# Performance work log

Hardware: AMD Instinct MI355X
Metric: run time of the kernel (lower is better)

The kernel has to match this reference:

```python
import jax, jax.numpy as jnp
import numpy as np

NUM_HEADS = 16

def _rope_tables(seq_len, head_dim, dtype):
    inv_freq = 1.0 / (10000.0 ** (jnp.arange(0, head_dim, 2, dtype=jnp.float32) / head_dim))
    t = jnp.arange(seq_len, dtype=jnp.float32)
    freqs = jnp.einsum('i,j->ij', t, inv_freq)          # [S, hd/2]
    emb = jnp.concatenate([freqs, freqs], axis=-1)      # [S, hd]
    return jnp.cos(emb).astype(dtype), jnp.sin(emb).astype(dtype)

def _rotate_half(x):
    x1, x2 = jnp.split(x, 2, axis=-1)
    return jnp.concatenate([-x2, x1], axis=-1)

def _apply_rope(x, cos, sin):
    # x: [B, H, S, hd]; cos/sin: [S, hd]
    return x * cos + _rotate_half(x) * sin

def setup_inputs() -> dict:
    key = jax.random.key(0)
    ks = jax.random.split(key, 9)
    S, B, E = 2048, 2, 1024
    sc_w = 1.0 / np.sqrt(E)
    inp = {
        'query': jax.random.normal(ks[0], (S, B, E), jnp.float32),
        'wq': jax.random.normal(ks[1], (E, E), jnp.float32) * sc_w,
        'bq': jax.random.normal(ks[2], (E,), jnp.float32) * 0.02,
        'wk': jax.random.normal(ks[3], (E, E), jnp.float32) * sc_w,
        'bk': jax.random.normal(ks[4], (E,), jnp.float32) * 0.02,
        'wv': jax.random.normal(ks[5], (E, E), jnp.float32) * sc_w,
        'bv': jax.random.normal(ks[6], (E,), jnp.float32) * 0.02,
        'wo': jax.random.normal(ks[7], (E, E), jnp.float32) * sc_w,
        'bo': jax.random.normal(ks[8], (E,), jnp.float32) * 0.02,
    }
    return inp

def reference(query, wq, bq, wk, bk, wv, bv, wo, bo):
    S, B, E = query.shape
    H = NUM_HEADS
    hd = E // H
    # QKV projections (torch Linear: x @ W^T + b). self_attention => k,v from query.
    q = jnp.einsum('sbe,fe->sbf', query, wq) + bq
    k = jnp.einsum('sbe,fe->sbf', query, wk) + bk
    v = jnp.einsum('sbe,fe->sbf', query, wv) + bv
    # [S, B, E] -> [B, H, S, hd]
    def to_bhsd(x):
        return x.reshape(S, B, H, hd).transpose(1, 2, 0, 3)
    q, k, v = to_bhsd(q), to_bhsd(k), to_bhsd(v)
    cos, sin = _rope_tables(S, hd, query.dtype)
    q = _apply_rope(q, cos, sin)
    k = _apply_rope(k, cos, sin)
    # scaled dot-product attention (no mask, no dropout)
    scale = 1.0 / jnp.sqrt(jnp.asarray(hd, query.dtype))
    scores = jnp.einsum('bhqd,bhkd->bhqk', q, k) * scale
    probs = jax.nn.softmax(scores, axis=-1)
    attn = jnp.einsum('bhqk,bhkd->bhqd', probs, v)
    # [B, H, S, hd] -> [S, B, E]
    attn = attn.transpose(2, 0, 1, 3).reshape(S, B, E)
    out = jnp.einsum('sbe,fe->sbf', attn, wo) + bo
    return out
```

## Files before the change

### kernel.cpp

```cpp
#include <hip/hip_runtime.h>
#include <stdint.h>

#define S_LEN 2048
#define BATCH 2
#define EMB   1024
#define NHEAD 16
#define HDIM  64

typedef __bf16 bf8   __attribute__((ext_vector_type(8)));
typedef float  f32x4 __attribute__((ext_vector_type(4)));
typedef float  f32x16 __attribute__((ext_vector_type(16)));

__device__ __forceinline__ unsigned short f2bf(float f) {
    unsigned u = __builtin_bit_cast(unsigned, f);
    u += 0x7fffu + ((u >> 16) & 1u);
    return (unsigned short)(u >> 16);
}
__device__ __forceinline__ float bf2f(unsigned short h) {
    unsigned u = ((unsigned)h) << 16;
    return __builtin_bit_cast(float, u);
}

__device__ __forceinline__ void gl_lds16(const unsigned short* g, unsigned short* l) {
    __builtin_amdgcn_global_load_lds(
        (__attribute__((address_space(1))) void*)(void*)g,
        (__attribute__((address_space(3))) void*)(void*)l, 16, 0, 0);
}

__global__ void k_tables(float* __restrict__ cosT, float* __restrict__ sinT) {
    int idx = blockIdx.x * 256 + threadIdx.x;
    int s = idx >> 6, d = idx & 63, j = d & 31;
    float inv = exp2f(-13.28771237954945f * ((float)j * (1.0f / 32.0f)));
    float ang = (float)s * inv;
    cosT[idx] = cosf(ang);
    sinT[idx] = sinf(ang);
}

__global__ void k_cast_x(const float* __restrict__ x, unsigned short* __restrict__ xb) {
    int id = blockIdx.x * 256 + threadIdx.x;
    int b = id >> 19, rem = id & 524287;
    int s = rem >> 8, e4 = (rem & 255) << 2;
    float4 v = *(const float4*)&x[((size_t)(s * BATCH + b)) * EMB + e4];
    ushort4 o;
    o.x = f2bf(v.x); o.y = f2bf(v.y); o.z = f2bf(v.z); o.w = f2bf(v.w);
    *(ushort4*)&xb[((size_t)(b * S_LEN + s)) * EMB + e4] = o;
}

__global__ void k_castW(const float* __restrict__ w0, const float* __restrict__ w1,
                        const float* __restrict__ w2, const float* __restrict__ w3,
                        unsigned short* __restrict__ o0, unsigned short* __restrict__ o1,
                        unsigned short* __restrict__ o2, unsigned short* __restrict__ o3) {
    int id = blockIdx.x * 256 + threadIdx.x;
    int seg = id >> 18, r = id & 262143;
    const float* s = seg == 0 ? w0 : seg == 1 ? w1 : seg == 2 ? w2 : w3;
    unsigned short* o = seg == 0 ? o0 : seg == 1 ? o1 : seg == 2 ? o2 : o3;
    float4 v = *(const float4*)&s[(size_t)r * 4];
    ushort4 u;
    u.x = f2bf(v.x); u.y = f2bf(v.y); u.z = f2bf(v.z); u.w = f2bf(v.w);
    *(ushort4*)&o[(size_t)r * 4] = u;
}

__global__ void __launch_bounds__(256) k_gemmQKV(
    const unsigned short* __restrict__ A,
    const unsigned short* __restrict__ Wq, const unsigned short* __restrict__ Wk,
    const unsigned short* __restrict__ Wv,
    const float* __restrict__ bqp, const float* __restrict__ bkp, const float* __restrict__ bvp,
    unsigned short* __restrict__ qout, unsigned short* __restrict__ kout,
    unsigned short* __restrict__ vout,
    const float* __restrict__ cosT, const float* __restrict__ sinT)
{
    __shared__ __align__(16) unsigned short As[128 * 32];
    __shared__ __align__(16) unsigned short Bs[128 * 32];
    const int z = blockIdx.z;
    const unsigned short* B = z == 0 ? Wq : z == 1 ? Wk : Wv;
    const float* bias = z == 0 ? bqp : z == 1 ? bkp : bvp;
    const int tid  = threadIdx.x;
    const int lane = tid & 63;
    const int wid  = tid >> 6;
    const int wm = wid >> 1, wn = wid & 1;
    const int l15 = lane & 15, lh = lane >> 4;
    const int tm0 = blockIdx.y * 128, tn0 = blockIdx.x * 128;
    const int K = 1024;

    f32x4 acc[4][4] = {};

    for (int k0 = 0; k0 < K; k0 += 32) {
        __syncthreads();
#pragma unroll
        for (int rnd = 0; rnd < 2; ++rnd) {
            int cbase = wid * 64 + rnd * 256;
            int c = cbase + lane;
            int row = c >> 2, co = (c & 3) * 8;
            gl_lds16(A + (size_t)(tm0 + row) * K + k0 + co, &As[cbase * 8]);
            gl_lds16(B + (size_t)(tn0 + row) * K + k0 + co, &Bs[cbase * 8]);
        }
        __syncthreads();
        bf8 a[4], b[4];
#pragma unroll
        for (int i = 0; i < 4; ++i) {
            a[i] = *(const bf8*)&As[(wm * 64 + i * 16 + l15) * 32 + lh * 8];
            b[i] = *(const bf8*)&Bs[(wn * 64 + i * 16 + l15) * 32 + lh * 8];
        }
#pragma unroll
        for (int i = 0; i < 4; ++i)
#pragma unroll
            for (int j = 0; j < 4; ++j)
                acc[i][j] = __builtin_amdgcn_mfma_f32_16x16x32_bf16(a[i], b[j], acc[i][j], 0, 0, 0);
    }

    if (z < 2) {
        unsigned short* C = z ? kout : qout;
        const float f = z ? 1.0f : 0.125f * 1.44269504089f;
#pragma unroll
        for (int i = 0; i < 4; ++i) {
            const int rowb = tm0 + wm * 64 + i * 16 + lh * 4;
#pragma unroll
            for (int j = 0; j < 2; ++j) {
                const int col = tn0 + wn * 64 + j * 16 + l15;
                const int d = j * 16 + l15;
#pragma unroll
                for (int r = 0; r < 4; ++r) {
                    int m = rowb + r;
                    int sq = m & (S_LEN - 1);
                    float x1 = acc[i][j][r]     + bias[col];
                    float x2 = acc[i][j + 2][r] + bias[col + 32];
                    float c  = cosT[sq * 64 + d] * f;
                    float sn = sinT[sq * 64 + d] * f;
                    C[(size_t)m * EMB + col]      = f2bf(x1 * c - x2 * sn);
                    C[(size_t)m * EMB + col + 32] = f2bf(x2 * c + x1 * sn);
                }
            }
        }
    } else {
#pragma unroll
        for (int i = 0; i < 4; ++i) {
            const int rowb = tm0 + wm * 64 + i * 16 + lh * 4;
#pragma unroll
            for (int j = 0; j < 4; ++j) {
                const int col = tn0 + wn * 64 + j * 16 + l15;
                float bv = bias[col];
#pragma unroll
                for (int r = 0; r < 4; ++r)
                    vout[(size_t)col * 4096 + rowb + r] = f2bf(acc[i][j][r] + bv);
            }
        }
    }
}

__global__ void __launch_bounds__(256) k_attn6(
    const unsigned short* __restrict__ qb,
    const unsigned short* __restrict__ kb,
    const unsigned short* __restrict__ vT,
    float* __restrict__ po0, float* __restrict__ po1,
    float* __restrict__ ml)
{
    __shared__ __align__(16) unsigned short Kl[2][4096];
    __shared__ __align__(16) unsigned short Vl[2][4096];
    __shared__ float bl[4][32];
    const int tid = threadIdx.x, lane = tid & 63, wid = tid >> 6;
    const int l31 = lane & 31, hi = lane >> 5;
    const int bh = blockIdx.y;
    const int b = bh >> 4, h = bh & 15;
    const int z = blockIdx.z;
    const int kv0 = z << 10;
    const int q0 = blockIdx.x * 128 + wid * 32;
    float* __restrict__ po = z ? po1 : po0;
    float* __restrict__ mlz = ml + (size_t)z * (32 * 2048 * 2);

    const unsigned short* qrow = qb + ((size_t)(b * S_LEN + q0 + l31)) * EMB + h * HDIM + hi * 8;
    bf8 qf[4];
#pragma unroll
    for (int c = 0; c < 4; ++c) qf[c] = *(const bf8*)(qrow + c * 16);

    const unsigned short* kb_g = kb + (size_t)b * S_LEN * EMB + h * HDIM;
    const unsigned short* vT_g = vT + (size_t)h * HDIM * (S_LEN * BATCH) + b * S_LEN;

    const int srow = lane >> 3;
    const int sp   = lane & 7;
    auto stage = [&](int buf, int j0) {
#pragma unroll
        for (int i = 0; i < 2; ++i) {
            int blk = wid * 2 + i;
            int r = blk * 8 + srow;
            int ps = sp ^ (r & 7);
            gl_lds16(kb_g + (size_t)(j0 + r) * EMB + ps * 8, &Kl[buf][blk * 512]);
            gl_lds16(vT_g + (size_t)r * (S_LEN * BATCH) + j0 + ps * 8, &Vl[buf][blk * 512]);
        }
    };

    auto pack2 = [](float lo, float hh) -> unsigned {
        unsigned short a  = __builtin_bit_cast(unsigned short, (__bf16)lo);
        unsigned short bb = __builtin_bit_cast(unsigned short, (__bf16)hh);
        return ((unsigned)bb << 16) | a;
    };

    float m_run = 0.f, l_run = 0.f;
    f32x16 oacc0 = {}, oacc1 = {};

    const int rA = l31, rB = 32 + l31;

    stage(0, kv0);
    __syncthreads();

    const int NT = 1024 / 64;
    for (int t = 0; t < NT; ++t) {
        const int cur = t & 1;
        if (t < NT - 1) stage(cur ^ 1, kv0 + (t + 1) * 64);

        f32x16 stA = {}, stB = {};
#pragma unroll
        for (int c = 0; c < 4; ++c) {
            int s = c * 2 + hi;
            bf8 kfa = *(const bf8*)&Kl[cur][rA * 64 + (s ^ (rA & 7)) * 8];
            bf8 kfb = *(const bf8*)&Kl[cur][rB * 64 + (s ^ (rB & 7)) * 8];
            stA = __builtin_amdgcn_mfma_f32_32x32x16_bf16(kfa, qf[c], stA, 0, 0, 0);
            stB = __builtin_amdgcn_mfma_f32_32x32x16_bf16(kfb, qf[c], stB, 0, 0, 0);
        }
        float mx[8];
#pragma unroll
        for (int i = 0; i < 8; ++i)
            mx[i] = fmaxf(fmaxf(stA[i], stA[i + 8]), fmaxf(stB[i], stB[i + 8]));
        float t0 = fmaxf(mx[0], mx[4]), t1 = fmaxf(mx[1], mx[5]);
        float t2 = fmaxf(mx[2], mx[6]), t3 = fmaxf(mx[3], mx[7]);
        float pmax = fmaxf(fmaxf(t0, t1), fmaxf(t2, t3));
        pmax = fmaxf(pmax, __shfl_xor(pmax, 32));
        if (!__all(pmax - m_run <= 11.54f)) {
            float mnew = fmaxf(m_run, pmax);
            float corr = exp2f(m_run - mnew);
            l_run *= corr;
            m_run = mnew;
            if (hi == 0) bl[wid][l31] = corr;
            asm volatile("s_waitcnt lgkmcnt(0)" ::: "memory");
#pragma unroll
            for (int r = 0; r < 16; ++r) {
                float c2 = bl[wid][(r & 3) + 8 * (r >> 2) + 4 * hi];
                oacc0[r] *= c2;
                oacc1[r] *= c2;
            }
        }
        float pA[16];
#pragma unroll
        for (int r = 0; r < 16; ++r) pA[r] = exp2f(stA[r] - m_run);
        float sA = ((pA[0] + pA[1]) + (pA[2] + pA[3])) + ((pA[4] + pA[5]) + (pA[6] + pA[7]));
        float sA2 = ((pA[8] + pA[9]) + (pA[10] + pA[11])) + ((pA[12] + pA[13]) + (pA[14] + pA[15]));
        unsigned a01 = pack2(pA[0], pA[1]),   a23 = pack2(pA[2], pA[3]);
        unsigned a45 = pack2(pA[4], pA[5]),   a67 = pack2(pA[6], pA[7]);
        unsigned a89 = pack2(pA[8], pA[9]),   aab = pack2(pA[10], pA[11]);
        unsigned acd = pack2(pA[12], pA[13]), aef = pack2(pA[14], pA[15]);
        unsigned rA_ = (unsigned)__shfl_xor((int)(hi ? a01 : a45), 32);
        unsigned rB_ = (unsigned)__shfl_xor((int)(hi ? a23 : a67), 32);
        unsigned rC_ = (unsigned)__shfl_xor((int)(hi ? a89 : acd), 32);
        unsigned rD_ = (unsigned)__shfl_xor((int)(hi ? aab : aef), 32);
        uint4 u0 = hi ? uint4{rA_, rB_, a45, a67} : uint4{a01, a23, rA_, rB_};
        uint4 u1 = hi ? uint4{rC_, rD_, acd, aef} : uint4{a89, aab, rC_, rD_};
        bf8 pf0A = __builtin_bit_cast(bf8, u0);
        bf8 pf1A = __builtin_bit_cast(bf8, u1);
        float pB[16];
#pragma unroll
        for (int r = 0; r < 16; ++r) pB[r] = exp2f(stB[r] - m_run);
        float sB = ((pB[0] + pB[1]) + (pB[2] + pB[3])) + ((pB[4] + pB[5]) + (pB[6] + pB[7]));
        float sB2 = ((pB[8] + pB[9]) + (pB[10] + pB[11])) + ((pB[12] + pB[13]) + (pB[14] + pB[15]));
        unsigned b01 = pack2(pB[0], pB[1]),   b23 = pack2(pB[2], pB[3]);
        unsigned b45 = pack2(pB[4], pB[5]),   b67 = pack2(pB[6], pB[7]);
        unsigned b89 = pack2(pB[8], pB[9]),   bab = pack2(pB[10], pB[11]);
        unsigned bcd = pack2(pB[12], pB[13]), bef = pack2(pB[14], pB[15]);
        unsigned sA_ = (unsigned)__shfl_xor((int)(hi ? b01 : b45), 32);
        unsigned sB_ = (unsigned)__shfl_xor((int)(hi ? b23 : b67), 32);
        unsigned sC_ = (unsigned)__shfl_xor((int)(hi ? b89 : bcd), 32);
        unsigned sD_ = (unsigned)__shfl_xor((int)(hi ? bab : bef), 32);
        uint4 w0 = hi ? uint4{sA_, sB_, b45, b67} : uint4{b01, b23, sA_, sB_};
        uint4 w1 = hi ? uint4{sC_, sD_, bcd, bef} : uint4{b89, bab, sC_, sD_};
        bf8 pf0B = __builtin_bit_cast(bf8, w0);
        bf8 pf1B = __builtin_bit_cast(bf8, w1);

        float psum = (sA + sA2) + (sB + sB2);
        psum += __shfl_xor(psum, 32);
        l_run += psum;

#pragma unroll
        for (int c = 0; c < 4; ++c) {
            int s = c * 2 + hi;
            bf8 v0 = *(const bf8*)&Vl[cur][rA * 64 + (s ^ (rA & 7)) * 8];
            bf8 v1 = *(const bf8*)&Vl[cur][rB * 64 + (s ^ (rB & 7)) * 8];
            bf8 pf = (c == 0) ? pf0A : (c == 1) ? pf1A : (c == 2) ? pf0B : pf1B;
            oacc0 = __builtin_amdgcn_mfma_f32_32x32x16_bf16(pf, v0, oacc0, 0, 0, 0);
            oacc1 = __builtin_amdgcn_mfma_f32_32x32x16_bf16(pf, v1, oacc1, 0, 0, 0);
        }
        __syncthreads();
    }

#pragma unroll
    for (int r = 0; r < 16; ++r) {
        int q = (r & 3) + 8 * (r >> 2) + 4 * hi;
        size_t base = ((size_t)bh * 2048 + q0 + q) * 64 + l31;
        po[base]      = oacc0[r];
        po[base + 32] = oacc1[r];
    }
    if (hi == 0) {
        size_t mi = ((size_t)bh * 2048 + q0 + l31) * 2;
        mlz[mi]     = m_run;
        mlz[mi + 1] = l_run;
    }
}

__global__ void k_comb(const float* __restrict__ po0, const float* __restrict__ po1,
                       const float* __restrict__ ml, unsigned short* __restrict__ ob)
{
    int id = blockIdx.x * 256 + threadIdx.x;
    int d4 = (id & 15) * 4;
    int q  = (id >> 4) & 2047;
    int bh = id >> 15;
    int b = bh >> 4, h = bh & 15;
    size_t mi = ((size_t)bh * 2048 + q) * 2;
    float m0 = ml[mi], l0 = ml[mi + 1];
    float m1 = ml[mi + (size_t)32 * 2048 * 2], l1 = ml[mi + (size_t)32 * 2048 * 2 + 1];
    float m = fmaxf(m0, m1);
    float w0 = exp2f(m0 - m), w1 = exp2f(m1 - m);
    float inv = 1.0f / (l0 * w0 + l1 * w1);
    size_t pi = ((size_t)bh * 2048 + q) * 64 + d4;
    float4 a = *(const float4*)&po0[pi];
    float4 c = *(const float4*)&po1[pi];
    ushort4 o;
    o.x = f2bf((a.x * w0 + c.x * w1) * inv);
    o.y = f2bf((a.y * w0 + c.y * w1) * inv);
    o.z = f2bf((a.z * w0 + c.z * w1) * inv);
    o.w = f2bf((a.w * w0 + c.w * w1) * inv);
    *(ushort4*)&ob[((size_t)(b * S_LEN + q)) * EMB + h * HDIM + d4] = o;
}

template<int EPI, typename OutT>
__global__ void __launch_bounds__(256) k_gemm(
    const unsigned short* __restrict__ A,
    const unsigned short* __restrict__ B,
    const float* __restrict__ bias,
    OutT* __restrict__ C,
    int M, int N, int K)
{
    __shared__ __align__(16) unsigned short As[128 * 32];
    __shared__ __align__(16) unsigned short Bs[128 * 32];
    const int tid  = threadIdx.x;
    const int lane = tid & 63;
    const int wid  = tid >> 6;
    const int wm = wid >> 1, wn = wid & 1;
    const int l15 = lane & 15, lh = lane >> 4;
    const int tm0 = blockIdx.y * 128, tn0 = blockIdx.x * 128;

    f32x4 acc[4][4] = {};

    for (int k0 = 0; k0 < K; k0 += 32) {
        __syncthreads();
#pragma unroll
        for (int rnd = 0; rnd < 2; ++rnd) {
            int cbase = wid * 64 + rnd * 256;
            int c = cbase + lane;
            int row = c >> 2, co = (c & 3) * 8;
            gl_lds16(A + (size_t)(tm0 + row) * K + k0 + co, &As[cbase * 8]);
            gl_lds16(B + (size_t)(tn0 + row) * K + k0 + co, &Bs[cbase * 8]);
        }
        __syncthreads();
        bf8 a[4], b[4];
#pragma unroll
        for (int i = 0; i < 4; ++i) {
            a[i] = *(const bf8*)&As[(wm * 64 + i * 16 + l15) * 32 + lh * 8];
            b[i] = *(const bf8*)&Bs[(wn * 64 + i * 16 + l15) * 32 + lh * 8];
        }
#pragma unroll
        for (int i = 0; i < 4; ++i)
#pragma unroll
            for (int j = 0; j < 4; ++j)
                acc[i][j] = __builtin_amdgcn_mfma_f32_16x16x32_bf16(a[i], b[j], acc[i][j], 0, 0, 0);
    }

#pragma unroll
    for (int i = 0; i < 4; ++i) {
        const int rowb = tm0 + wm * 64 + i * 16 + lh * 4;
#pragma unroll
        for (int j = 0; j < 4; ++j) {
            const int col = tn0 + wn * 64 + j * 16 + l15;
#pragma unroll
            for (int r = 0; r < 4; ++r) {
                float v = acc[i][j][r];
                int row = rowb + r;
                if (EPI == 0) {
                    v += bias[col];
                    C[(size_t)row * N + col] = (OutT)f2bf(v);
                } else {
                    v += bias[col];
                    int bb = row >> 11, ss = row & 2047;
                    ((float*)C)[(size_t)(ss * BATCH + bb) * N + col] = v;
                }
            }
        }
    }
}

extern "C" void kernel_launch(void* const* d_in, const int* in_sizes, int n_in,
                              void* d_out, int out_size, void* d_ws, size_t ws_size,
                              hipStream_t stream)
{
    (void)in_sizes; (void)n_in; (void)out_size; (void)ws_size;
    const float* query = (const float*)d_in[0];
    const float* wq = (const float*)d_in[1];
    const float* bq = (const float*)d_in[2];
    const float* wk = (const float*)d_in[3];
    const float* bk = (const float*)d_in[4];
    const float* wv = (const float*)d_in[5];
    const float* bv = (const float*)d_in[6];
    const float* wo = (const float*)d_in[7];
    const float* bo = (const float*)d_in[8];

    char* ws = (char*)d_ws;
    float*          cosT = (float*)(ws + 0);
    float*          sinT = (float*)(ws + (512 << 10));
    float*          ml   = (float*)(ws + 0);
    unsigned short* xb   = (unsigned short*)(ws + (1  << 20));
    float*          po0  = (float*)(ws + (1  << 20));
    unsigned short* wqb  = (unsigned short*)(ws + (9  << 20));
    unsigned short* wkb  = (unsigned short*)(ws + (11 << 20));
    unsigned short* wvb  = (unsigned short*)(ws + (13 << 20));
    unsigned short* qb   = (unsigned short*)(ws + (17 << 20));
    unsigned short* ob   = qb;
    unsigned short* kb   = (unsigned short*)(ws + (25 << 20));
    unsigned short* vT   = (unsigned short*)(ws + (33 << 20));
    float*          po1  = (float*)(ws + (41 << 20));
    unsigned short* wob  = (unsigned short*)(ws + (57 << 20));

    k_tables<<<512, 256, 0, stream>>>(cosT, sinT);
    k_cast_x<<<4096, 256, 0, stream>>>(query, xb);
    k_castW<<<4096, 256, 0, stream>>>(wq, wk, wv, wo, wqb, wkb, wvb, wob);

    dim3 gq(EMB / 128, (S_LEN * BATCH) / 128, 3);
    k_gemmQKV<<<gq, 256, 0, stream>>>(xb, wqb, wkb, wvb, bq, bk, bv,
                                      qb, kb, vT, cosT, sinT);

    dim3 g3(S_LEN / 128, BATCH * NHEAD, 2);
    k_attn6<<<g3, 256, 0, stream>>>(qb, kb, vT, po0, po1, ml);
    k_comb<<<4096, 256, 0, stream>>>(po0, po1, ml, ob);

    dim3 g1(EMB / 128, (S_LEN * BATCH) / 128);
    k_gemm<1, float><<<g1, 256, 0, stream>>>(ob, wob, bo, (float*)d_out, 4096, 1024, 1024);
}
```

Measured before the change: 184.1 us.

## Triple-buffer K/V staging in attention with vmcnt waits and MFMA priority

Replaces the double-buffered K/V LDS staging with a three-buffer ring. Each iteration waits with a partial vmcnt and one barrier, so two tiles stay in flight and the trailing per-iteration __syncthreads is gone. It also precomputes the swizzled LDS and global offsets, wraps the MFMA groups in s_setprio, and uses the raw hardware exp2 intrinsic in place of exp2f. The cost is more LDS per block (48KB), which may lower occupancy, plus hand-counted wait counts that must match the issued loads.

```diff
diff --git a/kernel.cpp b/kernel.cpp
--- a/kernel.cpp
+++ b/kernel.cpp
@@ -20,6 +20,8 @@
     unsigned u = ((unsigned)h) << 16;
     return __builtin_bit_cast(float, u);
 }
+__device__ __forceinline__ float fexp2(float x) { return __builtin_amdgcn_exp2f(x); }
+__device__ __forceinline__ float f3max(float a, float b, float c) { return fmaxf(fmaxf(a, b), c); }
 
 __device__ __forceinline__ void gl_lds16(const unsigned short* g, unsigned short* l) {
     __builtin_amdgcn_global_load_lds(
@@ -147,15 +149,14 @@
     }
 }
 
-__global__ void __launch_bounds__(256) k_attn6(
+__global__ void __launch_bounds__(256) k_attn8(
     const unsigned short* __restrict__ qb,
     const unsigned short* __restrict__ kb,
     const unsigned short* __restrict__ vT,
     float* __restrict__ po0, float* __restrict__ po1,
     float* __restrict__ ml)
 {
-    __shared__ __align__(16) unsigned short Kl[2][4096];
-    __shared__ __align__(16) unsigned short Vl[2][4096];
+    __shared__ __align__(16) unsigned short Sm[24576];
     __shared__ float bl[4][32];
     const int tid = threadIdx.x, lane = tid & 63, wid = tid >> 6;
     const int l31 = lane & 31, hi = lane >> 5;
@@ -172,21 +173,28 @@
 #pragma unroll
     for (int c = 0; c < 4; ++c) qf[c] = *(const bf8*)(qrow + c * 16);
 
-    const unsigned short* kb_g = kb + (size_t)b * S_LEN * EMB + h * HDIM;
-    const unsigned short* vT_g = vT + (size_t)h * HDIM * (S_LEN * BATCH) + b * S_LEN;
-
-    const int srow = lane >> 3;
-    const int sp   = lane & 7;
-    auto stage = [&](int buf, int j0) {
-#pragma unroll
-        for (int i = 0; i < 2; ++i) {
-            int blk = wid * 2 + i;
-            int r = blk * 8 + srow;
-            int ps = sp ^ (r & 7);
-            gl_lds16(kb_g + (size_t)(j0 + r) * EMB + ps * 8, &Kl[buf][blk * 512]);
-            gl_lds16(vT_g + (size_t)r * (S_LEN * BATCH) + j0 + ps * 8, &Vl[buf][blk * 512]);
-        }
-    };
+    const int mz = l31 & 7;
+    const int koA0 = l31 * 128 + (((0 * 2 + hi) ^ mz) << 4);
+    const int koA1 = l31 * 128 + (((1 * 2 + hi) ^ mz) << 4);
+    const int koA2 = l31 * 128 + (((2 * 2 + hi) ^ mz) << 4);
+    const int koA3 = l31 * 128 + (((3 * 2 + hi) ^ mz) << 4);
+    const char* ldsc = (const char*)Sm;
+
+    const int srow = lane >> 3, sp = lane & 7;
+    const int r0 = wid * 16 + srow,     p0s = sp ^ (r0 & 7);
+    const int r1 = wid * 16 + 8 + srow, p1s = sp ^ (r1 & 7);
+    const int kgo0 = (r0 * EMB + p0s * 8) * 2, kgo1 = (r1 * EMB + p1s * 8) * 2;
+    const int vgo0 = (r0 * (S_LEN * BATCH) + p0s * 8) * 2, vgo1 = (r1 * (S_LEN * BATCH) + p1s * 8) * 2;
+
+    const unsigned short* kS = kb + ((size_t)(b * S_LEN + kv0)) * EMB + h * HDIM;
+    const unsigned short* vS = vT + ((size_t)h * HDIM) * (S_LEN * BATCH) + b * S_LEN + kv0;
+
+#define STAGE8(DBUF) do { \
+    gl_lds16((const unsigned short*)((const char*)kS + kgo0), Sm + (DBUF) * 4096 + wid * 1024); \
+    gl_lds16((const unsigned short*)((const char*)vS + vgo0), Sm + 12288 + (DBUF) * 4096 + wid * 1024); \
+    gl_lds16((const unsigned short*)((const char*)kS + kgo1), Sm + (DBUF) * 4096 + wid * 1024 + 512); \
+    gl_lds16((const unsigned short*)((const char*)vS + vgo1), Sm + 12288 + (DBUF) * 4096 + wid * 1024 + 512); \
+    kS += 64 * EMB; vS += 64; } while (0)
 
     auto pack2 = [](float lo, float hh) -> unsigned {
         unsigned short a  = __builtin_bit_cast(unsigned short, (__bf16)lo);
@@ -196,98 +204,113 @@
 
     float m_run = 0.f, l_run = 0.f;
     f32x16 oacc0 = {}, oacc1 = {};
-
-    const int rA = l31, rB = 32 + l31;
-
-    stage(0, kv0);
-    __syncthreads();
-
-    const int NT = 1024 / 64;
-    for (int t = 0; t < NT; ++t) {
-        const int cur = t & 1;
-        if (t < NT - 1) stage(cur ^ 1, kv0 + (t + 1) * 64);
-
-        f32x16 stA = {}, stB = {};
-#pragma unroll
-        for (int c = 0; c < 4; ++c) {
-            int s = c * 2 + hi;
-            bf8 kfa = *(const bf8*)&Kl[cur][rA * 64 + (s ^ (rA & 7)) * 8];
-            bf8 kfb = *(const bf8*)&Kl[cur][rB * 64 + (s ^ (rB & 7)) * 8];
-            stA = __builtin_amdgcn_mfma_f32_32x32x16_bf16(kfa, qf[c], stA, 0, 0, 0);
-            stB = __builtin_amdgcn_mfma_f32_32x32x16_bf16(kfb, qf[c], stB, 0, 0, 0);
-        }
-        float mx[8];
-#pragma unroll
-        for (int i = 0; i < 8; ++i)
-            mx[i] = fmaxf(fmaxf(stA[i], stA[i + 8]), fmaxf(stB[i], stB[i + 8]));
-        float t0 = fmaxf(mx[0], mx[4]), t1 = fmaxf(mx[1], mx[5]);
-        float t2 = fmaxf(mx[2], mx[6]), t3 = fmaxf(mx[3], mx[7]);
-        float pmax = fmaxf(fmaxf(t0, t1), fmaxf(t2, t3));
-        pmax = fmaxf(pmax, __shfl_xor(pmax, 32));
-        if (!__all(pmax - m_run <= 11.54f)) {
-            float mnew = fmaxf(m_run, pmax);
-            float corr = exp2f(m_run - mnew);
-            l_run *= corr;
-            m_run = mnew;
-            if (hi == 0) bl[wid][l31] = corr;
-            asm volatile("s_waitcnt lgkmcnt(0)" ::: "memory");
-#pragma unroll
-            for (int r = 0; r < 16; ++r) {
-                float c2 = bl[wid][(r & 3) + 8 * (r >> 2) + 4 * hi];
-                oacc0[r] *= c2;
-                oacc1[r] *= c2;
-            }
-        }
-        float pA[16];
-#pragma unroll
-        for (int r = 0; r < 16; ++r) pA[r] = exp2f(stA[r] - m_run);
-        float sA = ((pA[0] + pA[1]) + (pA[2] + pA[3])) + ((pA[4] + pA[5]) + (pA[6] + pA[7]));
-        float sA2 = ((pA[8] + pA[9]) + (pA[10] + pA[11])) + ((pA[12] + pA[13]) + (pA[14] + pA[15]));
-        unsigned a01 = pack2(pA[0], pA[1]),   a23 = pack2(pA[2], pA[3]);
-        unsigned a45 = pack2(pA[4], pA[5]),   a67 = pack2(pA[6], pA[7]);
-        unsigned a89 = pack2(pA[8], pA[9]),   aab = pack2(pA[10], pA[11]);
-        unsigned acd = pack2(pA[12], pA[13]), aef = pack2(pA[14], pA[15]);
-        unsigned rA_ = (unsigned)__shfl_xor((int)(hi ? a01 : a45), 32);
-        unsigned rB_ = (unsigned)__shfl_xor((int)(hi ? a23 : a67), 32);
-        unsigned rC_ = (unsigned)__shfl_xor((int)(hi ? a89 : acd), 32);
-        unsigned rD_ = (unsigned)__shfl_xor((int)(hi ? aab : aef), 32);
-        uint4 u0 = hi ? uint4{rA_, rB_, a45, a67} : uint4{a01, a23, rA_, rB_};
-        uint4 u1 = hi ? uint4{rC_, rD_, acd, aef} : uint4{a89, aab, rC_, rD_};
-        bf8 pf0A = __builtin_bit_cast(bf8, u0);
-        bf8 pf1A = __builtin_bit_cast(bf8, u1);
-        float pB[16];
-#pragma unroll
-        for (int r = 0; r < 16; ++r) pB[r] = exp2f(stB[r] - m_run);
-        float sB = ((pB[0] + pB[1]) + (pB[2] + pB[3])) + ((pB[4] + pB[5]) + (pB[6] + pB[7]));
-        float sB2 = ((pB[8] + pB[9]) + (pB[10] + pB[11])) + ((pB[12] + pB[13]) + (pB[14] + pB[15]));
-        unsigned b01 = pack2(pB[0], pB[1]),   b23 = pack2(pB[2], pB[3]);
-        unsigned b45 = pack2(pB[4], pB[5]),   b67 = pack2(pB[6], pB[7]);
-        unsigned b89 = pack2(pB[8], pB[9]),   bab = pack2(pB[10], pB[11]);
-        unsigned bcd = pack2(pB[12], pB[13]), bef = pack2(pB[14], pB[15]);
-        unsigned sA_ = (unsigned)__shfl_xor((int)(hi ? b01 : b45), 32);
-        unsigned sB_ = (unsigned)__shfl_xor((int)(hi ? b23 : b67), 32);
-        unsigned sC_ = (unsigned)__shfl_xor((int)(hi ? b89 : bcd), 32);
-        unsigned sD_ = (unsigned)__shfl_xor((int)(hi ? bab : bef), 32);
-        uint4 w0 = hi ? uint4{sA_, sB_, b45, b67} : uint4{b01, b23, sA_, sB_};
-        uint4 w1 = hi ? uint4{sC_, sD_, bcd, bef} : uint4{b89, bab, sC_, sD_};
-        bf8 pf0B = __builtin_bit_cast(bf8, w0);
-        bf8 pf1B = __builtin_bit_cast(bf8, w1);
-
-        float psum = (sA + sA2) + (sB + sB2);
-        psum += __shfl_xor(psum, 32);
-        l_run += psum;
-
-#pragma unroll
-        for (int c = 0; c < 4; ++c) {
-            int s = c * 2 + hi;
-            bf8 v0 = *(const bf8*)&Vl[cur][rA * 64 + (s ^ (rA & 7)) * 8];
-            bf8 v1 = *(const bf8*)&Vl[cur][rB * 64 + (s ^ (rB & 7)) * 8];
-            bf8 pf = (c == 0) ? pf0A : (c == 1) ? pf1A : (c == 2) ? pf0B : pf1B;
-            oacc0 = __builtin_amdgcn_mfma_f32_32x32x16_bf16(pf, v0, oacc0, 0, 0, 0);
-            oacc1 = __builtin_amdgcn_mfma_f32_32x32x16_bf16(pf, v1, oacc1, 0, 0, 0);
-        }
-        __syncthreads();
-    }
+    const f32x16 Z16 = {};
+
+    STAGE8(0);
+    STAGE8(1);
+
+#define ABODY(BUF, DOSTG, LASTW) do { \
+    if (LASTW) asm volatile("s_waitcnt vmcnt(0)" ::: "memory"); \
+    else       asm volatile("s_waitcnt vmcnt(4)" ::: "memory"); \
+    __builtin_amdgcn_s_barrier(); \
+    if (DOSTG) STAGE8(((BUF) + 2) % 3); \
+    bf8 ka0 = *(const bf8*)(ldsc + koA0 + (BUF) * 8192); \
+    bf8 ka1 = *(const bf8*)(ldsc + koA1 + (BUF) * 8192); \
+    bf8 ka2 = *(const bf8*)(ldsc + koA2 + (BUF) * 8192); \
+    bf8 ka3 = *(const bf8*)(ldsc + koA3 + (BUF) * 8192); \
+    bf8 kb0 = *(const bf8*)(ldsc + koA0 + (BUF) * 8192 + 4096); \
+    bf8 kb1 = *(const bf8*)(ldsc + koA1 + (BUF) * 8192 + 4096); \
+    bf8 kb2 = *(const bf8*)(ldsc + koA2 + (BUF) * 8192 + 4096); \
+    bf8 kb3 = *(const bf8*)(ldsc + koA3 + (BUF) * 8192 + 4096); \
+    __builtin_amdgcn_s_setprio(1); \
+    f32x16 stA = __builtin_amdgcn_mfma_f32_32x32x16_bf16(ka0, qf[0], Z16, 0, 0, 0); \
+    f32x16 stB = __builtin_amdgcn_mfma_f32_32x32x16_bf16(kb0, qf[0], Z16, 0, 0, 0); \
+    stA = __builtin_amdgcn_mfma_f32_32x32x16_bf16(ka1, qf[1], stA, 0, 0, 0); \
+    stB = __builtin_amdgcn_mfma_f32_32x32x16_bf16(kb1, qf[1], stB, 0, 0, 0); \
+    stA = __builtin_amdgcn_mfma_f32_32x32x16_bf16(ka2, qf[2], stA, 0, 0, 0); \
+    stB = __builtin_amdgcn_mfma_f32_32x32x16_bf16(kb2, qf[2], stB, 0, 0, 0); \
+    stA = __builtin_amdgcn_mfma_f32_32x32x16_bf16(ka3, qf[3], stA, 0, 0, 0); \
+    stB = __builtin_amdgcn_mfma_f32_32x32x16_bf16(kb3, qf[3], stB, 0, 0, 0); \
+    __builtin_amdgcn_s_setprio(0); \
+    float g0 = f3max(f3max(stA[0], stA[1], stA[2]),  f3max(stA[3], stA[4], stA[5]),  f3max(stA[6], stA[7], stA[8])); \
+    float g1 = f3max(f3max(stA[9], stA[10], stA[11]), f3max(stA[12], stA[13], stA[14]), fmaxf(stA[15], stB[0])); \
+    float g2 = f3max(f3max(stB[1], stB[2], stB[3]),  f3max(stB[4], stB[5], stB[6]),  f3max(stB[7], stB[8], stB[9])); \
+    float g3 = f3max(f3max(stB[10], stB[11], stB[12]), f3max(stB[13], stB[14], stB[15]), fmaxf(g0, g1)); \
+    float pmax = f3max(g2, g3, g0); \
+    pmax = fmaxf(pmax, __shfl_xor(pmax, 32)); \
+    if (!__all(pmax - m_run <= 11.54f)) { \
+        float mnew = fmaxf(m_run, pmax); \
+        float corr = fexp2(m_run - mnew); \
+        l_run *= corr; m_run = mnew; \
+        if (hi == 0) bl[wid][l31] = corr; \
+        asm volatile("s_waitcnt lgkmcnt(0)" ::: "memory"); \
+        _Pragma("unroll") for (int r = 0; r < 16; ++r) { \
+            float c2 = bl[wid][(r & 3) + 8 * (r >> 2) + 4 * hi]; \
+            oacc0[r] *= c2; oacc1[r] *= c2; } \
+    } \
+    float pA[16], pB[16]; \
+    _Pragma("unroll") for (int r = 0; r < 16; ++r) pA[r] = fexp2(stA[r] - m_run); \
+    _Pragma("unroll") for (int r = 0; r < 16; ++r) pB[r] = fexp2(stB[r] - m_run); \
+    float sA = (((pA[0] + pA[1]) + (pA[2] + pA[3])) + ((pA[4] + pA[5]) + (pA[6] + pA[7]))) \
+             + (((pA[8] + pA[9]) + (pA[10] + pA[11])) + ((pA[12] + pA[13]) + (pA[14] + pA[15]))); \
+    float sB = (((pB[0] + pB[1]) + (pB[2] + pB[3])) + ((pB[4] + pB[5]) + (pB[6] + pB[7]))) \
+             + (((pB[8] + pB[9]) + (pB[10] + pB[11])) + ((pB[12] + pB[13]) + (pB[14] + pB[15]))); \
+    float psum = sA + sB; \
+    psum += __shfl_xor(psum, 32); \
+    l_run += psum; \
+    unsigned a0w = pack2(pA[0], pA[1]),  a1w = pack2(pA[2], pA[3]); \
+    unsigned a2w = pack2(pA[4], pA[5]),  a3w = pack2(pA[6], pA[7]); \
+    unsigned a4w = pack2(pA[8], pA[9]),  a5w = pack2(pA[10], pA[11]); \
+    unsigned a6w = pack2(pA[12], pA[13]), a7w = pack2(pA[14], pA[15]); \
+    unsigned rA_ = (unsigned)__shfl_xor((int)(hi ? a0w : a2w), 32); \
+    unsigned rB_ = (unsigned)__shfl_xor((int)(hi ? a1w : a3w), 32); \
+    unsigned rC_ = (unsigned)__shfl_xor((int)(hi ? a4w : a6w), 32); \
+    unsigned rD_ = (unsigned)__shfl_xor((int)(hi ? a5w : a7w), 32); \
+    uint4 uA0 = hi ? uint4{rA_, rB_, a2w, a3w} : uint4{a0w, a1w, rA_, rB_}; \
+    uint4 uA1 = hi ? uint4{rC_, rD_, a6w, a7w} : uint4{a4w, a5w, rC_, rD_}; \
+    bf8 pf0A = __builtin_bit_cast(bf8, uA0); \
+    bf8 pf1A = __builtin_bit_cast(bf8, uA1); \
+    unsigned b0w = pack2(pB[0], pB[1]),  b1w = pack2(pB[2], pB[3]); \
+    unsigned b2w = pack2(pB[4], pB[5]),  b3w = pack2(pB[6], pB[7]); \
+    unsigned b4w = pack2(pB[8], pB[9]),  b5w = pack2(pB[10], pB[11]); \
+    unsigned b6w = pack2(pB[12], pB[13]), b7w = pack2(pB[14], pB[15]); \
+    unsigned rE_ = (unsigned)__shfl_xor((int)(hi ? b0w : b2w), 32); \
+    unsigned rF_ = (unsigned)__shfl_xor((int)(hi ? b1w : b3w), 32); \
+    unsigned rG_ = (unsigned)__shfl_xor((int)(hi ? b4w : b6w), 32); \
+    unsigned rH_ = (unsigned)__shfl_xor((int)(hi ? b5w : b7w), 32); \
+    uint4 uB0 = hi ? uint4{rE_, rF_, b2w, b3w} : uint4{b0w, b1w, rE_, rF_}; \
+    uint4 uB1 = hi ? uint4{rG_, rH_, b6w, b7w} : uint4{b4w, b5w, rG_, rH_}; \
+    bf8 pf0B = __builtin_bit_cast(bf8, uB0); \
+    bf8 pf1B = __builtin_bit_cast(bf8, uB1); \
+    bf8 va0 = *(const bf8*)(ldsc + koA0 + 24576 + (BUF) * 8192); \
+    bf8 va1 = *(const bf8*)(ldsc + koA1 + 24576 + (BUF) * 8192); \
+    bf8 va2 = *(const bf8*)(ldsc + koA2 + 24576 + (BUF) * 8192); \
+    bf8 va3 = *(const bf8*)(ldsc + koA3 + 24576 + (BUF) * 8192); \
+    bf8 vb0 = *(const bf8*)(ldsc + koA0 + 24576 + (BUF) * 8192 + 4096); \
+    bf8 vb1 = *(const bf8*)(ldsc + koA1 + 24576 + (BUF) * 8192 + 4096); \
+    bf8 vb2 = *(const bf8*)(ldsc + koA2 + 24576 + (BUF) * 8192 + 4096); \
+    bf8 vb3 = *(const bf8*)(ldsc + koA3 + 24576 + (BUF) * 8192 + 4096); \
+    __builtin_amdgcn_s_setprio(1); \
+    oacc0 = __builtin_amdgcn_mfma_f32_32x32x16_bf16(pf0A, va0, oacc0, 0, 0, 0); \
+    oacc1 = __builtin_amdgcn_mfma_f32_32x32x16_bf16(pf0A, vb0, oacc1, 0, 0, 0); \
+    oacc0 = __builtin_amdgcn_mfma_f32_32x32x16_bf16(pf1A, va1, oacc0, 0, 0, 0); \
+    oacc1 = __builtin_amdgcn_mfma_f32_32x32x16_bf16(pf1A, vb1, oacc1, 0, 0, 0); \
+    oacc0 = __builtin_amdgcn_mfma_f32_32x32x16_bf16(pf0B, va2, oacc0, 0, 0, 0); \
+    oacc1 = __builtin_amdgcn_mfma_f32_32x32x16_bf16(pf0B, vb2, oacc1, 0, 0, 0); \
+    oacc0 = __builtin_amdgcn_mfma_f32_32x32x16_bf16(pf1B, va3, oacc0, 0, 0, 0); \
+    oacc1 = __builtin_amdgcn_mfma_f32_32x32x16_bf16(pf1B, vb3, oacc1, 0, 0, 0); \
+    __builtin_amdgcn_s_setprio(0); \
+} while (0)
+
+    for (int t3 = 0; t3 < 5; ++t3) {
+        ABODY(0, true, false);
+        ABODY(1, true, false);
+        ABODY(2, (t3 < 4), false);
+    }
+    ABODY(0, false, true);
+
+#undef ABODY
+#undef STAGE8
 
 #pragma unroll
     for (int r = 0; r < 16; ++r) {
@@ -315,7 +338,7 @@
     float m0 = ml[mi], l0 = ml[mi + 1];
     float m1 = ml[mi + (size_t)32 * 2048 * 2], l1 = ml[mi + (size_t)32 * 2048 * 2 + 1];
     float m = fmaxf(m0, m1);
-    float w0 = exp2f(m0 - m), w1 = exp2f(m1 - m);
+    float w0 = fexp2(m0 - m), w1 = fexp2(m1 - m);
     float inv = 1.0f / (l0 * w0 + l1 * w1);
     size_t pi = ((size_t)bh * 2048 + q) * 64 + d4;
     float4 a = *(const float4*)&po0[pi];
@@ -434,7 +457,7 @@
                                       qb, kb, vT, cosT, sinT);
 
     dim3 g3(S_LEN / 128, BATCH * NHEAD, 2);
-    k_attn6<<<g3, 256, 0, stream>>>(qb, kb, vT, po0, po1, ml);
+    k_attn8<<<g3, 256, 0, stream>>>(qb, kb, vT, po0, po1, ml);
     k_comb<<<4096, 256, 0, stream>>>(po0, po1, ml, ob);
 
     dim3 g1(EMB / 128, (S_LEN * BATCH) / 128);
```

Result: faster. 168.0 us (-8.7%).
